# Kernel tuning notes

Hardware: AMD Instinct MI355X
Metric: run time of the kernel (lower is better)

## Reference

```python
import jax, jax.numpy as jnp
import numpy as np

INFTY_APPROX = 1e30
LAM = 10000.0


def sinusoid_embs(length, width):
    # Transformer-XL sinusoidal embeddings, flipped so row 0 encodes the
    # largest relative distance (length-1), matching the rel_shift convention.
    pos = jnp.arange(length, dtype=jnp.float32)
    inv_lams = 1.0 / (LAM ** (jnp.arange(0, width, 2, dtype=jnp.float32) / width))
    pre = pos[:, None] * inv_lams[None, :]                 # [T, width//2]
    cat = jnp.concatenate([jnp.sin(pre), jnp.cos(pre)], axis=-1)  # [T, width]
    return jnp.flip(cat, axis=0)


def rel_shift(x):
    # x: [B, T, T] -> out[b,i,j] = x[b, i, j - i + T - 1] (XL pad/reshape trick)
    b, t, _ = x.shape
    x = jnp.pad(x, ((0, 0), (0, 0), (1, 0)))               # [B, T, T+1]
    x = x.reshape(b, t + 1, t)[:, 1:, :]                   # [B, T, T]
    return x


def setup_inputs() -> dict:
    B, T, D, K, V = 2, 4096, 1024, 128, 2048
    key = jax.random.key(0)
    ks = jax.random.split(key, 10)
    s_d = 1.0 / np.sqrt(D)
    s_v = 1.0 / np.sqrt(V)
    return {
        'x':    jax.random.normal(ks[0], (B, T, D), dtype=jnp.float32),
        'g_ln': jnp.ones((D,), dtype=jnp.float32),
        'W_q':  s_d * jax.random.normal(ks[1], (D, K), dtype=jnp.float32),
        'W_k':  s_d * jax.random.normal(ks[2], (D, K), dtype=jnp.float32),
        'W_v':  s_d * jax.random.normal(ks[3], (D, V), dtype=jnp.float32),
        'W_g':  s_d * jax.random.normal(ks[4], (D, V), dtype=jnp.float32),
        'W_r':  s_d * jax.random.normal(ks[5], (D, K), dtype=jnp.float32),
        'xl_u': 0.02 * jax.random.normal(ks[6], (K,), dtype=jnp.float32),
        'xl_v': 0.02 * jax.random.normal(ks[7], (K,), dtype=jnp.float32),
        'W_o':  s_v * jax.random.normal(ks[8], (V, D), dtype=jnp.float32),
    }


def reference(x, g_ln, W_q, W_k, W_v, W_g, W_r, xl_u, xl_v, W_o):
    B, T, D = x.shape
    K = W_q.shape[-1]
    tau = jnp.asarray(K, x.dtype) ** 0.5

    # RMSNorm input layernorm
    x_tilde = x * jax.lax.rsqrt(jnp.mean(jnp.square(x), axis=-1, keepdims=True) + 1e-6)
    x_tilde = x_tilde * g_ln

    # QKVG projections; queries pre-scaled by 1/tau (producer-side scaling)
    q = (x_tilde @ W_q) / tau                              # [B, T, K]
    k = x_tilde @ W_k                                      # [B, T, K]
    v = x_tilde @ W_v                                      # [B, T, V]

    # XL relative-position bias inputs
    xl_r = sinusoid_embs(T, D) @ W_r                       # [T, K]

    # AC term (content) and BD term (position) with XL u/v biases
    scores_ac = jnp.einsum('bik,bjk->bij', q + xl_u, k)    # [B, T, T]
    scores_bd = jnp.einsum('bik,jk->bij', q + xl_v, xl_r)  # [B, T, T]
    scores_bd = rel_shift(scores_bd)

    scores = scores_ac + scores_bd
    keep = jnp.tril(jnp.ones((T, T), dtype=bool))          # causal keep mask
    scores = scores - jnp.asarray(INFTY_APPROX, x.dtype) * jnp.logical_not(keep)

    w = jax.nn.softmax(scores, axis=-1)                    # [B, T, T]
    wv = jnp.einsum('bij,bjv->biv', w, v)                  # [B, T, V]

    # SHGA gating (GAU-style silu gate)
    wv = wv * jax.nn.silu(x_tilde @ W_g)

    res = wv @ W_o                                         # [B, T, D]
    return res
```

## Files before the change

### kernel.cpp

```cpp
#include <hip/hip_runtime.h>
#include <hip/hip_bf16.h>
#include <stdint.h>

typedef __attribute__((ext_vector_type(4))) float f32x4;
typedef __attribute__((ext_vector_type(8))) short s16x8;
typedef __attribute__((ext_vector_type(8))) unsigned short u16x8;
typedef __attribute__((ext_vector_type(4))) unsigned short u16x4;

static __device__ __forceinline__ float b2f(unsigned short u) {
  union { unsigned int i; float f; } v; v.i = ((unsigned int)u) << 16; return v.f;
}
static __device__ __forceinline__ unsigned short f2b(float f) {
  unsigned int x = __float_as_uint(f);
  return (unsigned short)((x + 0x7fffu + ((x >> 16) & 1u)) >> 16);
}

typedef __attribute__((address_space(1))) const void gconst_t;
typedef __attribute__((address_space(3))) void lds_t;
static __device__ __forceinline__ void gload_lds16(const void* g, void* l) {
  __builtin_amdgcn_global_load_lds((gconst_t*)g, (lds_t*)l, 16, 0, 0);
}

template<int N>
static __device__ __forceinline__ void vmwait() {
  asm volatile("s_waitcnt vmcnt(%0)" :: "n"(N) : "memory");
}

struct GemmP {
  const unsigned short* A; const unsigned short* B; void* C;
  long sA, sB, sC;
  int M, N, K, lda, ldb, ldc;
  int causal, kend_mode;
  int gxs, gys, qchunk;
  const float* uvec; const float* vvec;
  unsigned short* qv_out; unsigned short* kk_out; float invtau;
  const float* rinv; const unsigned short* gate;
  const unsigned short* bds; float* stats;
};

template<int NREP, int EPI>
__launch_bounds__(512, 4)
__global__ void gemm2p_k(GemmP p) {
  constexpr int BN = NREP * 64;
  constexpr int CB = NREP / 2;
  constexpr int LPT = 1 + CB;
  const int lin = (int)blockIdx.x + (((int)blockIdx.y + (int)blockIdx.z * (int)gridDim.y) << p.gxs);
  const int wg = (lin & 7) * p.qchunk + (lin >> 3);
  int ii = wg & ((1 << p.gxs) - 1);
  const int jj = (wg >> p.gxs) & ((1 << p.gys) - 1);
  const int b  = wg >> (p.gxs + p.gys);
  if (p.kend_mode) ii = (1 << p.gxs) - 1 - ii;
  const int i0 = ii * 128, j0 = jj * BN;
  if (p.causal && j0 > i0 + 127) return;
  const unsigned short* Ag = p.A + (long)b * p.sA + (long)i0 * p.lda;
  const unsigned short* Bg = p.B + (long)b * p.sB + (long)j0 * p.ldb;
  const int kend = p.kend_mode ? min(p.K, i0 + 128) : p.K;
  const int NT = kend >> 5;

  __shared__ unsigned short As[3][128 * 32];
  __shared__ unsigned short Bs[3][BN * 32];

  const int tid = threadIdx.x;
  const int w = tid >> 6, l = tid & 63;
  const int wr = w >> 2, wc = w & 3;
  const int lrow = l >> 2;
  const int swz = ((l & 3) ^ ((l >> 3) & 3)) * 8;

  auto stage = [&](int t, int bi) {
    gload_lds16((const void*)(Ag + (long)(w * 16 + lrow) * p.lda + t * 32 + swz),
                (void*)(&As[bi][w * 512]));
#pragma unroll
    for (int i = 0; i < CB; ++i) {
      const int c = w * CB + i;
      gload_lds16((const void*)(Bg + (long)(c * 16 + lrow) * p.ldb + t * 32 + swz),
                  (void*)(&Bs[bi][c * 512]));
    }
  };

  f32x4 acc[4][NREP];
#pragma unroll
  for (int m = 0; m < 4; ++m)
#pragma unroll
    for (int n = 0; n < NREP; ++n) acc[m][n] = (f32x4){0.f, 0.f, 0.f, 0.f};

  const int fr = l & 15, fq = l >> 4;
  const int rg = (fq ^ ((fr >> 1) & 3)) * 8;
  const int aoff = (wr * 64 + fr) * 32 + rg;
  const int boff = (wc * (NREP * 16) + fr) * 32 + rg;

  stage(0, 0);
  if (NT > 1) stage(1, 1);

  int bi = 0;
  for (int t = 0; t < NT; ++t) {
    if (t == NT - 1) vmwait<0>(); else vmwait<LPT>();
    __builtin_amdgcn_s_barrier();
    __builtin_amdgcn_sched_barrier(0);
    const unsigned short* as = &As[bi][0];
    const unsigned short* bs = &Bs[bi][0];
    s16x8 af[4], bf[NREP];
#pragma unroll
    for (int m = 0; m < 4; ++m) af[m] = *(const s16x8*)(as + aoff + m * 512);
#pragma unroll
    for (int n = 0; n < NREP; ++n) bf[n] = *(const s16x8*)(bs + boff + n * 512);
    if (t + 2 < NT) {
      int bi2 = bi + 2; if (bi2 >= 3) bi2 -= 3;
      stage(t + 2, bi2);
    }
    __builtin_amdgcn_s_setprio(1);
#pragma unroll
    for (int m = 0; m < 4; ++m)
#pragma unroll
      for (int n = 0; n < NREP; ++n)
        acc[m][n] = __builtin_amdgcn_mfma_f32_16x16x32_bf16(af[m], bf[n], acc[m][n], 0, 0, 0);
    __builtin_amdgcn_s_setprio(0);
    bi = (bi + 1 == 3) ? 0 : bi + 1;
  }

  const int rbase = i0 + wr * 64 + fq * 4;
  const int cbase = j0 + wc * (NREP * 16) + fr;
  const long tb = (long)b * p.sC;

  if constexpr (EPI == 6) {
    float ps[16];
#pragma unroll
    for (int t = 0; t < 16; ++t) ps[t] = 0.f;
#pragma unroll
    for (int m = 0; m < 4; ++m) {
#pragma unroll
      for (int n = 0; n < NREP; ++n) {
        const int col = cbase + n * 16;
#pragma unroll
        for (int e = 0; e < 4; ++e) {
          const int row = rbase + m * 16 + e;
          const long o = tb + (long)row * p.ldc + col;
          float ev = 0.f;
          if (col <= row) {
            const float s = acc[m][n][e] + b2f(p.bds[o]);
            ev = __expf(fminf(s, 60.f));
          }
          ((unsigned short*)p.C)[o] = f2b(ev);
          ps[m * 4 + e] += ev;
        }
      }
    }
#pragma unroll
    for (int t = 0; t < 16; ++t) {
      float v = ps[t];
      v += __shfl_xor(v, 1); v += __shfl_xor(v, 2);
      v += __shfl_xor(v, 4); v += __shfl_xor(v, 8);
      ps[t] = v;
    }
    if (fr == 0) {
#pragma unroll
      for (int t = 0; t < 16; ++t) {
        const int row = rbase + (t >> 2) * 16 + (t & 3);
        p.stats[((long)(b * p.M + row) * 16 + jj) * 4 + wc] = ps[t];
      }
    }
    return;
  }

#pragma unroll
  for (int m = 0; m < 4; ++m) {
#pragma unroll
    for (int n = 0; n < NREP; ++n) {
      const int col = cbase + n * 16;
#pragma unroll
      for (int e = 0; e < 4; ++e) {
        const int row = rbase + m * 16 + e;
        const float val = acc[m][n][e];
        if constexpr (EPI == 0) {
          ((unsigned short*)p.C)[tb + (long)row * p.ldc + col] = f2b(val);
        } else if constexpr (EPI == 1) {
          ((float*)p.C)[tb + (long)row * p.ldc + col] = val;
        } else if constexpr (EPI == 2) {
          ((unsigned short*)p.C)[tb + (long)row * p.ldc + col] =
              f2b(val / (1.f + __expf(-val)));
        } else if constexpr (EPI == 4) {
          const long coff = tb + (long)row * p.ldc + col;
          const float g = b2f(p.gate[coff]);
          const float r = p.rinv[b * p.M + row];
          ((unsigned short*)p.C)[coff] = f2b(val * r * g);
        } else if constexpr (EPI == 5) {
          if (col <= row)
            ((unsigned short*)p.C)[tb + (long)row * p.ldc + (row - col)] = f2b(val);
        }
      }
    }
  }
}

template<int EPI>
__launch_bounds__(256)
__global__ void gemm_bt_k(GemmP p) {
  const int i0 = blockIdx.x * 128;
  const int j0 = blockIdx.y * 128;
  const int b  = blockIdx.z;
  const unsigned short* A = p.A + (long)b * p.sA + (long)i0 * p.lda;
  const unsigned short* B = p.B + (long)b * p.sB + (long)j0 * p.ldb;
  const int kend = p.K;

  __shared__ unsigned short As[128 * 32];
  __shared__ unsigned short Bs[128 * 32];

  const int tid = threadIdx.x;
  const int w = tid >> 6, l = tid & 63;
  const int wr = w >> 1, wc = w & 1;

  f32x4 acc[4][4];
#pragma unroll
  for (int m = 0; m < 4; ++m)
#pragma unroll
    for (int n = 0; n < 4; ++n) acc[m][n] = (f32x4){0.f, 0.f, 0.f, 0.f};

  const int srow = (l >> 2);
  const int scol = ((l & 3) ^ ((l >> 3) & 3)) * 8;
  const unsigned short* ga0 = A + (long)(w * 16 + srow) * p.lda + scol;
  const unsigned short* ga1 = A + (long)((w + 4) * 16 + srow) * p.lda + scol;
  const unsigned short* gb0 = B + (long)(w * 16 + srow) * p.ldb + scol;
  const unsigned short* gb1 = B + (long)((w + 4) * 16 + srow) * p.ldb + scol;
  unsigned short* la0 = As + w * 512;
  unsigned short* la1 = As + (w + 4) * 512;
  unsigned short* lb0 = Bs + w * 512;
  unsigned short* lb1 = Bs + (w + 4) * 512;

  const int rg = ((l >> 4) ^ (((l & 15) >> 1) & 3)) * 8;
  const unsigned short* ap = As + ((wr * 64) + (l & 15)) * 32 + rg;
  const unsigned short* bp = Bs + ((wc * 64) + (l & 15)) * 32 + rg;

  for (int k0 = 0; k0 < kend; k0 += 32) {
    gload_lds16(ga0 + k0, la0);
    gload_lds16(ga1 + k0, la1);
    gload_lds16(gb0 + k0, lb0);
    gload_lds16(gb1 + k0, lb1);
    __syncthreads();
    s16x8 af[4], bfr[4];
#pragma unroll
    for (int m = 0; m < 4; ++m) af[m] = *(const s16x8*)(ap + m * 16 * 32);
#pragma unroll
    for (int n = 0; n < 4; ++n) bfr[n] = *(const s16x8*)(bp + n * 16 * 32);
#pragma unroll
    for (int m = 0; m < 4; ++m)
#pragma unroll
      for (int n = 0; n < 4; ++n)
        acc[m][n] = __builtin_amdgcn_mfma_f32_16x16x32_bf16(af[m], bfr[n], acc[m][n], 0, 0, 0);
    __syncthreads();
  }

  const int rbase = i0 + wr * 64 + (l >> 4) * 4;
  const int cbase = j0 + wc * 64 + (l & 15);
#pragma unroll
  for (int m = 0; m < 4; ++m) {
#pragma unroll
    for (int n = 0; n < 4; ++n) {
      const int col = cbase + n * 16;
#pragma unroll
      for (int e = 0; e < 4; ++e) {
        const int row = rbase + m * 16 + e;
        const float val = acc[m][n][e];
        if constexpr (EPI == 0) {
          ((unsigned short*)p.C)[(long)b * p.sC + (long)row * p.ldc + col] = f2b(val);
        } else if constexpr (EPI == 3) {
          if (j0 == 0) {
            const float q = val * p.invtau;
            const long o = (long)row * 128 + col;
            ((unsigned short*)p.C)[o] = f2b(q + p.uvec[col]);
            p.qv_out[o] = f2b(q + p.vvec[col]);
          } else {
            p.kk_out[(long)row * 128 + (col - 128)] = f2b(val);
          }
        }
      }
    }
  }
}

__launch_bounds__(256)
__global__ void rmsnorm_k(const float* __restrict__ x, const float* __restrict__ g,
                          unsigned short* __restrict__ xt) {
  const long row = blockIdx.x;
  const float* xr = x + row * 1024;
  const int t = threadIdx.x;
  const float4 v = ((const float4*)xr)[t];
  float ss = v.x * v.x + v.y * v.y + v.z * v.z + v.w * v.w;
#pragma unroll
  for (int o = 1; o < 64; o <<= 1) ss += __shfl_xor(ss, o);
  __shared__ float wsum[4];
  if ((t & 63) == 0) wsum[t >> 6] = ss;
  __syncthreads();
  const float tot = wsum[0] + wsum[1] + wsum[2] + wsum[3];
  const float r = 1.0f / sqrtf(tot * (1.0f / 1024.0f) + 1e-6f);
  const float4 gv = ((const float4*)g)[t];
  u16x4 o;
  o.x = f2b(v.x * r * gv.x); o.y = f2b(v.y * r * gv.y);
  o.z = f2b(v.z * r * gv.z); o.w = f2b(v.w * r * gv.w);
  ((u16x4*)(xt + row * 1024))[t] = o;
}

__launch_bounds__(256)
__global__ void sinemb_k(unsigned short* __restrict__ emb) {
  const int idx = blockIdx.x * 256 + threadIdx.x;
  const int t = idx >> 10, w = idx & 1023;
  const int h = w & 511;
  const float inv = __expf(-(float)h * (9.2103403719761836f / 512.0f));
  const float pre = (float)t * inv;
  const float val = (w < 512) ? sinf(pre) : cosf(pre);
  emb[idx] = f2b(val);
}

__launch_bounds__(256)
__global__ void transcast_k(const float* __restrict__ in, unsigned short* __restrict__ out,
                            int R, int C) {
  __shared__ float tile[32][33];
  const int c0 = blockIdx.x * 32, r0 = blockIdx.y * 32;
  const int tx = threadIdx.x & 31, ty = threadIdx.x >> 5;
#pragma unroll
  for (int k = 0; k < 4; ++k)
    tile[ty + k * 8][tx] = in[(long)(r0 + ty + k * 8) * C + c0 + tx];
  __syncthreads();
#pragma unroll
  for (int k = 0; k < 4; ++k)
    out[(long)(c0 + ty + k * 8) * R + r0 + tx] = f2b(tile[tx][ty + k * 8]);
}

__global__ void rowinv_k(const float* __restrict__ stats, float* __restrict__ rinv,
                         int T, int BT) {
  const int idx = blockIdx.x * 256 + threadIdx.x;
  if (idx >= BT) return;
  const int i = idx & (T - 1);
  const int nt = (i >> 8) + 1;
  const float* st = stats + (long)idx * 64;
  float s = 0.f;
  for (int jt = 0; jt < nt; ++jt)
    s += st[jt * 4] + st[jt * 4 + 1] + st[jt * 4 + 2] + st[jt * 4 + 3];
  rinv[idx] = 1.0f / s;
}

extern "C" void kernel_launch(void* const* d_in, const int* in_sizes, int n_in,
                              void* d_out, int out_size, void* d_ws, size_t ws_size,
                              hipStream_t stream) {
  const float* x    = (const float*)d_in[0];
  const float* g_ln = (const float*)d_in[1];
  const float* W_q  = (const float*)d_in[2];
  const float* W_k  = (const float*)d_in[3];
  const float* W_v  = (const float*)d_in[4];
  const float* W_g  = (const float*)d_in[5];
  const float* W_r  = (const float*)d_in[6];
  const float* xl_u = (const float*)d_in[7];
  const float* xl_v = (const float*)d_in[8];
  const float* W_o  = (const float*)d_in[9];
  float* out = (float*)d_out;

  const int B = 2, T = 4096, D = 1024, K = 128, V = 2048;
  const int BT = B * T;

  char* ws = (char*)d_ws;
  size_t off = 0;
  auto alloc = [&](size_t bytes) -> void* {
    void* p = ws + off; off += (bytes + 255) & ~(size_t)255; return p;
  };
  unsigned short* XT   = (unsigned short*)alloc((size_t)BT * D * 2);
  unsigned short* WQKT = (unsigned short*)alloc((size_t)256 * D * 2);
  unsigned short* WVT  = (unsigned short*)alloc((size_t)V * D * 2);
  unsigned short* WGT  = (unsigned short*)alloc((size_t)V * D * 2);
  unsigned short* WRT  = (unsigned short*)alloc((size_t)K * D * 2);
  unsigned short* WOT  = (unsigned short*)alloc((size_t)D * V * 2);
  unsigned short* QU   = (unsigned short*)alloc((size_t)BT * K * 2);
  unsigned short* QV   = (unsigned short*)alloc((size_t)BT * K * 2);
  unsigned short* KKb  = (unsigned short*)alloc((size_t)BT * K * 2);
  unsigned short* RR   = (unsigned short*)alloc((size_t)T * K * 2);
  unsigned short* VVT  = (unsigned short*)alloc((size_t)V * BT * 2);
  unsigned short* GATE = (unsigned short*)alloc((size_t)BT * V * 2);
  float* STATS         = (float*)alloc((size_t)BT * 64 * 4);
  float* RINV          = (float*)alloc((size_t)BT * 4);
  unsigned short* EBUF = (unsigned short*)alloc((size_t)B * T * T * 2);
  unsigned short* BD2  = (unsigned short*)alloc((size_t)B * T * T * 2);
  unsigned short* EMB  = BD2;
  unsigned short* WVG  = BD2;
  if (off > ws_size) return;
  (void)in_sizes; (void)n_in; (void)out_size;

  const float invtau = 0.08838834764831845f;

  transcast_k<<<dim3(K / 32, D / 32), 256, 0, stream>>>(W_q, WQKT, D, K);
  transcast_k<<<dim3(K / 32, D / 32), 256, 0, stream>>>(W_k, WQKT + (size_t)K * D, D, K);
  transcast_k<<<dim3(V / 32, D / 32), 256, 0, stream>>>(W_v, WVT, D, V);
  transcast_k<<<dim3(V / 32, D / 32), 256, 0, stream>>>(W_g, WGT, D, V);
  transcast_k<<<dim3(K / 32, D / 32), 256, 0, stream>>>(W_r, WRT, D, K);
  transcast_k<<<dim3(D / 32, V / 32), 256, 0, stream>>>(W_o, WOT, V, D);
  rmsnorm_k<<<BT, 256, 0, stream>>>(x, g_ln, XT);
  sinemb_k<<<(T * D) / 256, 256, 0, stream>>>(EMB);

  {
    GemmP p{}; p.A = XT; p.B = WQKT; p.C = QU;
    p.M = BT; p.N = 256; p.K = D; p.lda = D; p.ldb = D; p.ldc = K;
    p.uvec = xl_u; p.vvec = xl_v; p.qv_out = QV; p.kk_out = KKb; p.invtau = invtau;
    gemm_bt_k<3><<<dim3(BT / 128, 2, 1), 256, 0, stream>>>(p);
  }
  {
    GemmP p{}; p.A = EMB; p.B = WRT; p.C = RR;
    p.M = T; p.N = K; p.K = D; p.lda = D; p.ldb = D; p.ldc = K;
    gemm_bt_k<0><<<dim3(T / 128, 1, 1), 256, 0, stream>>>(p);
  }
  {
    GemmP p{}; p.A = WVT; p.B = XT; p.C = VVT;
    p.M = V; p.N = BT; p.K = D; p.lda = D; p.ldb = D; p.ldc = BT;
    p.gxs = 4; p.gys = 5; p.qchunk = 64;
    gemm2p_k<4, 0><<<dim3(16, 32, 1), 512, 0, stream>>>(p);
  }
  {
    GemmP p{}; p.A = XT; p.B = WGT; p.C = GATE;
    p.M = BT; p.N = V; p.K = D; p.lda = D; p.ldb = D; p.ldc = V;
    p.gxs = 6; p.gys = 3; p.qchunk = 64;
    gemm2p_k<4, 2><<<dim3(64, 8, 1), 512, 0, stream>>>(p);
  }
  {
    GemmP p{}; p.A = QV; p.B = RR; p.C = BD2;
    p.sA = (long)T * K; p.sB = 0; p.sC = (long)T * T;
    p.M = T; p.N = T; p.K = K; p.lda = K; p.ldb = K; p.ldc = T; p.causal = 1;
    p.gxs = 5; p.gys = 4; p.qchunk = 128;
    gemm2p_k<4, 5><<<dim3(32, 16, B), 512, 0, stream>>>(p);
  }
  {
    GemmP p{}; p.A = QU; p.B = KKb; p.C = EBUF;
    p.sA = (long)T * K; p.sB = (long)T * K; p.sC = (long)T * T;
    p.M = T; p.N = T; p.K = K; p.lda = K; p.ldb = K; p.ldc = T; p.causal = 1;
    p.bds = BD2; p.stats = STATS;
    p.gxs = 5; p.gys = 4; p.qchunk = 128;
    gemm2p_k<4, 6><<<dim3(32, 16, B), 512, 0, stream>>>(p);
  }
  rowinv_k<<<BT / 256, 256, 0, stream>>>(STATS, RINV, T, BT);
  {
    GemmP p{}; p.A = EBUF; p.B = VVT; p.C = WVG;
    p.sA = (long)T * T; p.sB = T; p.sC = (long)T * V;
    p.M = T; p.N = V; p.K = T; p.lda = T; p.ldb = BT; p.ldc = V;
    p.kend_mode = 1; p.rinv = RINV; p.gate = GATE;
    p.gxs = 5; p.gys = 3; p.qchunk = 64;
    gemm2p_k<4, 4><<<dim3(32, 8, B), 512, 0, stream>>>(p);
  }
  {
    GemmP p{}; p.A = WVG; p.B = WOT; p.C = out;
    p.M = BT; p.N = D; p.K = V; p.lda = V; p.ldb = V; p.ldc = D;
    p.gxs = 6; p.gys = 3; p.qchunk = 64;
    gemm2p_k<2, 1><<<dim3(64, 8, 1), 512, 0, stream>>>(p);
  }
}
```

Measured before the change: 408.8 us.

## Add larger-tile 4-stage pipelined GEMM kernel for V, gate, PV and output projections

```diff
diff --git a/kernel.cpp b/kernel.cpp
--- a/kernel.cpp
+++ b/kernel.cpp
@@ -24,6 +24,10 @@
 template<int N>
 static __device__ __forceinline__ void vmwait() {
   asm volatile("s_waitcnt vmcnt(%0)" :: "n"(N) : "memory");
+}
+static __device__ __forceinline__ void lgkm0() {
+  asm volatile("s_waitcnt lgkmcnt(0)" ::: "memory");
+  __builtin_amdgcn_sched_barrier(0);
 }
 
 struct GemmP {
@@ -37,6 +41,145 @@
   const float* rinv; const unsigned short* gate;
   const unsigned short* bds; float* stats;
 };
+
+template<int WM, int WN, int MFR, int NFR, int EPI>
+__launch_bounds__(512, 2)
+__global__ void gemm3_k(GemmP p) {
+  constexpr int BM = WM * MFR * 16;
+  constexpr int BN = WN * NFR * 16;
+  constexpr int LA = BM / 128;
+  constexpr int LB = BN / 128;
+  constexpr int LPT = LA + LB;
+  const int lin = (int)blockIdx.x + (((int)blockIdx.y + (int)blockIdx.z * (int)gridDim.y) << p.gxs);
+  const int wg = (lin & 7) * p.qchunk + (lin >> 3);
+  int ii = wg & ((1 << p.gxs) - 1);
+  const int jj = (wg >> p.gxs) & ((1 << p.gys) - 1);
+  const int b  = wg >> (p.gxs + p.gys);
+  if (p.kend_mode) ii = (1 << p.gxs) - 1 - ii;
+  const int i0 = ii * BM, j0 = jj * BN;
+  const unsigned short* Ag = p.A + (long)b * p.sA + (long)i0 * p.lda;
+  const unsigned short* Bg = p.B + (long)b * p.sB + (long)j0 * p.ldb;
+  const int kend = p.kend_mode ? min(p.K, i0 + BM) : p.K;
+  const int NT = kend >> 5;
+
+  __shared__ unsigned short As[4][BM * 32];
+  __shared__ unsigned short Bs[4][BN * 32];
+
+  const int tid = threadIdx.x;
+  const int w = tid >> 6, l = tid & 63;
+  const int wr = w / WN, wc = w % WN;
+
+  auto stageA = [&](int t, int s) {
+#pragma unroll
+    for (int j = 0; j < LA; ++j) {
+      const int sl = j * 512 + tid;
+      const int r = sl >> 2, g = sl & 3;
+      gload_lds16((const void*)(Ag + (long)r * p.lda + t * 32 + ((g ^ ((r >> 1) & 3)) << 3)),
+                  (void*)(&As[s][sl << 3]));
+    }
+  };
+  auto stageB = [&](int t, int s) {
+#pragma unroll
+    for (int j = 0; j < LB; ++j) {
+      const int sl = j * 512 + tid;
+      const int r = sl >> 2, g = sl & 3;
+      gload_lds16((const void*)(Bg + (long)r * p.ldb + t * 32 + ((g ^ ((r >> 1) & 3)) << 3)),
+                  (void*)(&Bs[s][sl << 3]));
+    }
+  };
+
+  f32x4 acc[MFR][NFR];
+#pragma unroll
+  for (int m = 0; m < MFR; ++m)
+#pragma unroll
+    for (int n = 0; n < NFR; ++n) acc[m][n] = (f32x4){0.f, 0.f, 0.f, 0.f};
+
+  const int fr = l & 15, fq = l >> 4;
+  const int rg = (fq ^ ((fr >> 1) & 3)) << 3;
+  const int aoff = (wr * (MFR * 16) + fr) * 32 + rg;
+  const int boff = (wc * (NFR * 16) + fr) * 32 + rg;
+
+  if (NT > 0) { stageA(0, 0); stageB(0, 0); }
+  if (NT > 1) { stageA(1, 1); stageB(1, 1); }
+  if (NT > 2) { stageA(2, 2); stageB(2, 2); }
+
+  constexpr int H = (MFR == 8) ? 4 : MFR;
+
+  for (int t = 0; t < NT; ++t) {
+    const int s = t & 3;
+    const int rem = NT - 1 - t;
+    if (rem >= 2)      vmwait<2 * LPT>();
+    else if (rem == 1) vmwait<LPT>();
+    else               vmwait<0>();
+    __builtin_amdgcn_s_barrier();
+    __builtin_amdgcn_sched_barrier(0);
+    const unsigned short* as = &As[s][0];
+    const unsigned short* bs = &Bs[s][0];
+    const int s3 = (t + 3) & 3;
+    const bool pf = (t + 3 < NT);
+
+    s16x8 bf[NFR];
+#pragma unroll
+    for (int n = 0; n < NFR; ++n) bf[n] = *(const s16x8*)(bs + boff + n * 512);
+    s16x8 af0[H];
+#pragma unroll
+    for (int m = 0; m < H; ++m) af0[m] = *(const s16x8*)(as + aoff + m * 512);
+    if (pf) stageA(t + 3, s3);
+    if constexpr (MFR != 8) { if (pf) stageB(t + 3, s3); }
+    lgkm0();
+    __builtin_amdgcn_s_setprio(1);
+#pragma unroll
+    for (int m = 0; m < H; ++m)
+#pragma unroll
+      for (int n = 0; n < NFR; ++n)
+        acc[m][n] = __builtin_amdgcn_mfma_f32_16x16x32_bf16(af0[m], bf[n], acc[m][n], 0, 0, 0);
+    __builtin_amdgcn_s_setprio(0);
+
+    if constexpr (MFR == 8) {
+      s16x8 af1[4];
+#pragma unroll
+      for (int m = 0; m < 4; ++m) af1[m] = *(const s16x8*)(as + aoff + (m + 4) * 512);
+      if (pf) stageB(t + 3, s3);
+      lgkm0();
+      __builtin_amdgcn_s_setprio(1);
+#pragma unroll
+      for (int m = 0; m < 4; ++m)
+#pragma unroll
+        for (int n = 0; n < NFR; ++n)
+          acc[m + 4][n] = __builtin_amdgcn_mfma_f32_16x16x32_bf16(af1[m], bf[n], acc[m + 4][n], 0, 0, 0);
+      __builtin_amdgcn_s_setprio(0);
+    }
+  }
+
+  const int rbase = i0 + wr * (MFR * 16) + fq * 4;
+  const int cbase = j0 + wc * (NFR * 16) + fr;
+  const long tb = (long)b * p.sC;
+#pragma unroll
+  for (int m = 0; m < MFR; ++m) {
+#pragma unroll
+    for (int n = 0; n < NFR; ++n) {
+      const int col = cbase + n * 16;
+#pragma unroll
+      for (int e = 0; e < 4; ++e) {
+        const int row = rbase + m * 16 + e;
+        const float val = acc[m][n][e];
+        if constexpr (EPI == 0) {
+          ((unsigned short*)p.C)[tb + (long)row * p.ldc + col] = f2b(val);
+        } else if constexpr (EPI == 1) {
+          ((float*)p.C)[tb + (long)row * p.ldc + col] = val;
+        } else if constexpr (EPI == 2) {
+          ((unsigned short*)p.C)[tb + (long)row * p.ldc + col] =
+              f2b(val / (1.f + __expf(-val)));
+        } else if constexpr (EPI == 4) {
+          const long coff = tb + (long)row * p.ldc + col;
+          const float g = b2f(p.gate[coff]);
+          const float r = p.rinv[b * p.M + row];
+          ((unsigned short*)p.C)[coff] = f2b(val * r * g);
+        }
+      }
+    }
+  }
+}
 
 template<int NREP, int EPI>
 __launch_bounds__(512, 4)
@@ -170,19 +313,7 @@
       for (int e = 0; e < 4; ++e) {
         const int row = rbase + m * 16 + e;
         const float val = acc[m][n][e];
-        if constexpr (EPI == 0) {
-          ((unsigned short*)p.C)[tb + (long)row * p.ldc + col] = f2b(val);
-        } else if constexpr (EPI == 1) {
-          ((float*)p.C)[tb + (long)row * p.ldc + col] = val;
-        } else if constexpr (EPI == 2) {
-          ((unsigned short*)p.C)[tb + (long)row * p.ldc + col] =
-              f2b(val / (1.f + __expf(-val)));
-        } else if constexpr (EPI == 4) {
-          const long coff = tb + (long)row * p.ldc + col;
-          const float g = b2f(p.gate[coff]);
-          const float r = p.rinv[b * p.M + row];
-          ((unsigned short*)p.C)[coff] = f2b(val * r * g);
-        } else if constexpr (EPI == 5) {
+        if constexpr (EPI == 5) {
           if (col <= row)
             ((unsigned short*)p.C)[tb + (long)row * p.ldc + (row - col)] = f2b(val);
         }
@@ -406,14 +537,14 @@
   {
     GemmP p{}; p.A = WVT; p.B = XT; p.C = VVT;
     p.M = V; p.N = BT; p.K = D; p.lda = D; p.ldb = D; p.ldc = BT;
-    p.gxs = 4; p.gys = 5; p.qchunk = 64;
-    gemm2p_k<4, 0><<<dim3(16, 32, 1), 512, 0, stream>>>(p);
+    p.gxs = 3; p.gys = 5; p.qchunk = 32;
+    gemm3_k<2, 4, 8, 4, 0><<<dim3(8, 32, 1), 512, 0, stream>>>(p);
   }
   {
     GemmP p{}; p.A = XT; p.B = WGT; p.C = GATE;
     p.M = BT; p.N = V; p.K = D; p.lda = D; p.ldb = D; p.ldc = V;
-    p.gxs = 6; p.gys = 3; p.qchunk = 64;
-    gemm2p_k<4, 2><<<dim3(64, 8, 1), 512, 0, stream>>>(p);
+    p.gxs = 5; p.gys = 3; p.qchunk = 32;
+    gemm3_k<2, 4, 8, 4, 2><<<dim3(32, 8, 1), 512, 0, stream>>>(p);
   }
   {
     GemmP p{}; p.A = QV; p.B = RR; p.C = BD2;
@@ -436,13 +567,13 @@
     p.sA = (long)T * T; p.sB = T; p.sC = (long)T * V;
     p.M = T; p.N = V; p.K = T; p.lda = T; p.ldb = BT; p.ldc = V;
     p.kend_mode = 1; p.rinv = RINV; p.gate = GATE;
-    p.gxs = 5; p.gys = 3; p.qchunk = 64;
-    gemm2p_k<4, 4><<<dim3(32, 8, B), 512, 0, stream>>>(p);
+    p.gxs = 4; p.gys = 4; p.qchunk = 64;
+    gemm3_k<4, 2, 4, 4, 4><<<dim3(16, 16, B), 512, 0, stream>>>(p);
   }
   {
     GemmP p{}; p.A = WVG; p.B = WOT; p.C = out;
     p.M = BT; p.N = D; p.K = V; p.lda = V; p.ldb = V; p.ldc = D;
-    p.gxs = 6; p.gys = 3; p.qchunk = 64;
-    gemm2p_k<2, 1><<<dim3(64, 8, 1), 512, 0, stream>>>(p);
-  }
-}
+    p.gxs = 5; p.gys = 3; p.qchunk = 32;
+    gemm3_k<4, 2, 4, 4, 1><<<dim3(32, 8, 1), 512, 0, stream>>>(p);
+  }
+}
```

After: 461.6 us. 12.9% more time.

## Add 8-wave 256-tile GEMM kernels with paired causal row blocks for projections and PV

Applied to the files above, without the earlier changes.

```diff
diff --git a/kernel.cpp b/kernel.cpp
--- a/kernel.cpp
+++ b/kernel.cpp
@@ -25,18 +25,288 @@
 static __device__ __forceinline__ void vmwait() {
   asm volatile("s_waitcnt vmcnt(%0)" :: "n"(N) : "memory");
 }
+static __device__ __forceinline__ void barmid() {
+  __builtin_amdgcn_sched_barrier(0);
+  __builtin_amdgcn_s_barrier();
+  asm volatile("s_waitcnt lgkmcnt(0)" ::: "memory");
+  __builtin_amdgcn_sched_barrier(0);
+}
+static __device__ __forceinline__ void barend() {
+  __builtin_amdgcn_sched_barrier(0);
+  __builtin_amdgcn_s_barrier();
+}
 
 struct GemmP {
   const unsigned short* A; const unsigned short* B; void* C;
   long sA, sB, sC;
   int M, N, K, lda, ldb, ldc;
-  int causal, kend_mode;
+  int causal, kend_mode, swapxy;
   int gxs, gys, qchunk;
   const float* uvec; const float* vvec;
   unsigned short* qv_out; unsigned short* kk_out; float invtau;
   const float* rinv; const unsigned short* gate;
   const unsigned short* bds; float* stats;
 };
+
+template<int EPI>
+__launch_bounds__(512, 2)
+__global__ void gemm8p256_k(GemmP p) {
+  __shared__ unsigned short L[2][4][8192];
+  const int lin = (int)blockIdx.x + (int)gridDim.x * ((int)blockIdx.y + (int)gridDim.y * (int)blockIdx.z);
+  const int wg = (lin & 7) * p.qchunk + (lin >> 3);
+  const int xx = wg & ((1 << p.gxs) - 1);
+  const int yy = (wg >> p.gxs) & ((1 << p.gys) - 1);
+  const int ii = p.swapxy ? yy : xx;
+  const int jj = p.swapxy ? xx : yy;
+  const int i0 = ii * 256, j0 = jj * 256;
+  const unsigned short* Ag = p.A + (long)i0 * p.lda;
+  const unsigned short* Bg = p.B + (long)j0 * p.ldb;
+  const int lda = p.lda, ldb = p.ldb;
+  const int NI = p.K >> 7;
+
+  const int tid = threadIdx.x;
+  const int w = tid >> 6, l = tid & 63;
+  const int wr = w >> 2, wc = w & 3;
+  const int fr = l & 15, fq = l >> 4;
+
+  auto stA = [&](int slot, int h, int t) {
+#pragma unroll
+    for (int u = 0; u < 2; ++u) {
+      const int sl = u * 512 + tid, r = sl >> 3, g = sl & 7;
+      const int gs = g ^ (((r >> 2) & 1) << 1);
+      gload_lds16(Ag + (long)(h * 128 + r) * lda + t * 64 + gs * 8, &L[slot][h][sl * 8]);
+    }
+  };
+  auto stB = [&](int slot, int h, int t) {
+#pragma unroll
+    for (int u = 0; u < 2; ++u) {
+      const int sl = u * 512 + tid, r = sl >> 3, g = sl & 7;
+      const int gs = g ^ (((r >> 2) & 1) << 1);
+      gload_lds16(Bg + (long)(h * 128 + r) * ldb + t * 64 + gs * 8, &L[slot][2 + h][sl * 8]);
+    }
+  };
+
+  f32x4 acc[8][4];
+#pragma unroll
+  for (int m = 0; m < 8; ++m)
+#pragma unroll
+    for (int n = 0; n < 4; ++n) acc[m][n] = (f32x4){0.f, 0.f, 0.f, 0.f};
+
+  const int abase = (((fr << 7) + (fq << 4)) ^ ((fr & 4) << 3));
+  const int bbase = ((((wc & 1) << 13) + (fr << 7) + (fq << 4)) ^ ((fr & 4) << 3));
+  s16x8 a[4][2], bA[2][2], bB[2][2];
+
+  auto rdA = [&](int slot, int mq) {
+#pragma unroll
+    for (int m = 0; m < 4; ++m)
+#pragma unroll
+      for (int ks = 0; ks < 2; ++ks)
+        a[m][ks] = *(const s16x8*)((const char*)&L[slot][wr][0] +
+                                   (abase | ((mq * 4 + m) << 11) | (ks << 6)));
+  };
+  auto rdB = [&](int slot, int nq, s16x8 (&bb)[2][2]) {
+    const int reg = 2 + (wc >> 1);
+#pragma unroll
+    for (int n = 0; n < 2; ++n)
+#pragma unroll
+      for (int ks = 0; ks < 2; ++ks)
+        bb[n][ks] = *(const s16x8*)((const char*)&L[slot][reg][0] +
+                                    (bbase | ((nq * 2 + n) << 11) | (ks << 6)));
+  };
+  auto mm = [&](int mq, int nq, s16x8 (&bb)[2][2]) {
+    __builtin_amdgcn_s_setprio(1);
+#pragma unroll
+    for (int m = 0; m < 4; ++m)
+#pragma unroll
+      for (int n = 0; n < 2; ++n)
+#pragma unroll
+        for (int ks = 0; ks < 2; ++ks)
+          acc[mq * 4 + m][nq * 2 + n] =
+              __builtin_amdgcn_mfma_f32_16x16x32_bf16(a[m][ks], bb[n][ks],
+                                                      acc[mq * 4 + m][nq * 2 + n], 0, 0, 0);
+    __builtin_amdgcn_s_setprio(0);
+  };
+
+  stB(0, 0, 0); stB(0, 1, 0); stA(0, 0, 0); stA(0, 1, 0);
+  stB(1, 0, 1); stB(1, 1, 1);
+  vmwait<4>();
+  barend();
+
+  for (int it = 0; it < NI; ++it) {
+    const int t0 = 2 * it, t1 = t0 + 1;
+    const bool lastI = (it == NI - 1);
+    rdA(0, 0); rdB(0, 0, bA); stA(1, 0, t1);
+    barmid(); mm(0, 0, bA); barend();
+    rdB(0, 1, bB); stA(1, 1, t1);
+    barmid(); mm(0, 1, bB); barend();
+    rdA(0, 1);
+    if (!lastI) stB(0, 0, t0 + 2);
+    barmid(); mm(1, 1, bB); barend();
+    if (!lastI) stB(0, 1, t0 + 2);
+    barmid(); mm(1, 0, bA);
+    if (lastI) vmwait<0>(); else vmwait<4>();
+    barend();
+    rdA(1, 0); rdB(1, 0, bA);
+    if (!lastI) stA(0, 0, t0 + 2);
+    barmid(); mm(0, 0, bA); barend();
+    rdB(1, 1, bB);
+    if (!lastI) stA(0, 1, t0 + 2);
+    barmid(); mm(0, 1, bB); barend();
+    rdA(1, 1);
+    if (!lastI) stB(1, 0, t1 + 2);
+    barmid(); mm(1, 1, bB); barend();
+    if (!lastI) stB(1, 1, t1 + 2);
+    barmid(); mm(1, 0, bA);
+    if (!lastI) vmwait<4>();
+    barend();
+  }
+
+  const int rb = i0 + wr * 128 + fq * 4;
+  const int cb = j0 + wc * 64 + fr;
+#pragma unroll
+  for (int m = 0; m < 8; ++m)
+#pragma unroll
+    for (int n = 0; n < 4; ++n) {
+      const int col = cb + n * 16;
+#pragma unroll
+      for (int e = 0; e < 4; ++e) {
+        const int row = rb + m * 16 + e;
+        const float val = acc[m][n][e];
+        if constexpr (EPI == 0)
+          ((unsigned short*)p.C)[(long)row * p.ldc + col] = f2b(val);
+        else
+          ((unsigned short*)p.C)[(long)row * p.ldc + col] = f2b(val / (1.f + __expf(-val)));
+      }
+    }
+}
+
+template<int PAIR, int EPI>
+__launch_bounds__(512, 2)
+__global__ void gemm8p128_k(GemmP p) {
+  __shared__ unsigned short L[3][3][8192];
+  const int lin = (int)blockIdx.x + (int)gridDim.x * ((int)blockIdx.y + (int)gridDim.y * (int)blockIdx.z);
+  const int wg = (lin & 7) * p.qchunk + (lin >> 3);
+  const int xx = wg & ((1 << p.gxs) - 1);
+  const int yy = (wg >> p.gxs) & ((1 << p.gys) - 1);
+  const int b  = wg >> (p.gxs + p.gys);
+  const int jj = PAIR ? yy : (p.swapxy ? xx : yy);
+  const int j0 = jj * 128;
+  const unsigned short* Bg0 = p.B + (long)b * p.sB + (long)j0 * p.ldb;
+  const int lda = p.lda, ldb = p.ldb;
+
+  const int tid = threadIdx.x;
+  const int w = tid >> 6, l = tid & 63;
+  const int wr = w >> 1, wc = w & 1;
+  const int fr = l & 15, fq = l >> 4;
+
+  const int abase = ((((wr & 1) << 13) + (fr << 7) + (fq << 4)) ^ ((fr & 4) << 3));
+  const int bbase = (((wc << 13) + (fr << 7) + (fq << 4)) ^ ((fr & 4) << 3));
+
+  const int passes = PAIR ? 2 : 1;
+  for (int ps = 0; ps < passes; ++ps) {
+    const int ii = PAIR ? (ps ? xx : (15 - xx)) : (p.swapxy ? yy : xx);
+    const int i0 = ii * 256;
+    const unsigned short* Ag = p.A + (long)b * p.sA + (long)i0 * lda;
+    const int kend = p.kend_mode ? min(p.K, i0 + 256) : p.K;
+    const int NT = kend >> 6;
+
+    auto stA = [&](int slot, int h, int t) {
+#pragma unroll
+      for (int u = 0; u < 2; ++u) {
+        const int sl = u * 512 + tid, r = sl >> 3, g = sl & 7;
+        const int gs = g ^ (((r >> 2) & 1) << 1);
+        gload_lds16(Ag + (long)(h * 128 + r) * lda + t * 64 + gs * 8, &L[slot][h][sl * 8]);
+      }
+    };
+    auto stB = [&](int slot, int bh, int t) {
+      const int r = tid >> 3, g = tid & 7;
+      const int rloc = bh * 64 + r;
+      const int gs = g ^ (((rloc >> 2) & 1) << 1);
+      gload_lds16(Bg0 + (long)rloc * ldb + t * 64 + gs * 8, &L[slot][2][bh * 4096 + tid * 8]);
+    };
+
+    f32x4 acc[4][4];
+#pragma unroll
+    for (int m = 0; m < 4; ++m)
+#pragma unroll
+      for (int n = 0; n < 4; ++n) acc[m][n] = (f32x4){0.f, 0.f, 0.f, 0.f};
+    s16x8 a[4][2], bA[2][2], bB[2][2];
+
+    auto rdA = [&](int slot) {
+      const int reg = wr >> 1;
+#pragma unroll
+      for (int m = 0; m < 4; ++m)
+#pragma unroll
+        for (int ks = 0; ks < 2; ++ks)
+          a[m][ks] = *(const s16x8*)((const char*)&L[slot][reg][0] +
+                                     (abase | (m << 11) | (ks << 6)));
+    };
+    auto rdB = [&](int slot, int nq, s16x8 (&bb)[2][2]) {
+#pragma unroll
+      for (int n = 0; n < 2; ++n)
+#pragma unroll
+        for (int ks = 0; ks < 2; ++ks)
+          bb[n][ks] = *(const s16x8*)((const char*)&L[slot][2][0] +
+                                      (bbase | ((nq * 2 + n) << 11) | (ks << 6)));
+    };
+    auto mm = [&](int nq, s16x8 (&bb)[2][2]) {
+      __builtin_amdgcn_s_setprio(1);
+#pragma unroll
+      for (int m = 0; m < 4; ++m)
+#pragma unroll
+        for (int n = 0; n < 2; ++n)
+#pragma unroll
+          for (int ks = 0; ks < 2; ++ks)
+            acc[m][nq * 2 + n] =
+                __builtin_amdgcn_mfma_f32_16x16x32_bf16(a[m][ks], bb[n][ks],
+                                                        acc[m][nq * 2 + n], 0, 0, 0);
+      __builtin_amdgcn_s_setprio(0);
+    };
+
+    stA(0, 0, 0); stB(0, 0, 0); stA(0, 1, 0); stB(0, 1, 0);
+    stA(1, 0, 1); stB(1, 0, 1); stA(1, 1, 1); stB(1, 1, 1);
+    vmwait<6>();
+    barend();
+
+    int s = 0;
+    for (int t = 0; t < NT; ++t) {
+      int s2 = s + 2; if (s2 >= 3) s2 -= 3;
+      const bool pf = (t + 2 < NT);
+      rdA(s); rdB(s, 0, bA);
+      if (pf) { stA(s2, 0, t + 2); stB(s2, 0, t + 2); }
+      barmid(); mm(0, bA); barend();
+      rdB(s, 1, bB);
+      if (pf) { stA(s2, 1, t + 2); stB(s2, 1, t + 2); }
+      barmid(); mm(1, bB);
+      if (t == NT - 2) vmwait<0>(); else if (t < NT - 2) vmwait<6>();
+      barend();
+      s = (s + 1 == 3) ? 0 : s + 1;
+    }
+
+    const int rb = i0 + wr * 64 + fq * 4;
+    const int cb = j0 + wc * 64 + fr;
+    const long tb = (long)b * p.sC;
+#pragma unroll
+    for (int m = 0; m < 4; ++m)
+#pragma unroll
+      for (int n = 0; n < 4; ++n) {
+        const int col = cb + n * 16;
+#pragma unroll
+        for (int e = 0; e < 4; ++e) {
+          const int row = rb + m * 16 + e;
+          const float val = acc[m][n][e];
+          if constexpr (EPI == 1) {
+            ((float*)p.C)[tb + (long)row * p.ldc + col] = val;
+          } else {
+            const long coff = tb + (long)row * p.ldc + col;
+            const float g = b2f(p.gate[coff]);
+            const float r = p.rinv[b * p.M + row];
+            ((unsigned short*)p.C)[coff] = f2b(val * r * g);
+          }
+        }
+      }
+  }
+}
 
 template<int NREP, int EPI>
 __launch_bounds__(512, 4)
@@ -46,16 +316,14 @@
   constexpr int LPT = 1 + CB;
   const int lin = (int)blockIdx.x + (((int)blockIdx.y + (int)blockIdx.z * (int)gridDim.y) << p.gxs);
   const int wg = (lin & 7) * p.qchunk + (lin >> 3);
-  int ii = wg & ((1 << p.gxs) - 1);
+  const int ii = wg & ((1 << p.gxs) - 1);
   const int jj = (wg >> p.gxs) & ((1 << p.gys) - 1);
   const int b  = wg >> (p.gxs + p.gys);
-  if (p.kend_mode) ii = (1 << p.gxs) - 1 - ii;
   const int i0 = ii * 128, j0 = jj * BN;
   if (p.causal && j0 > i0 + 127) return;
   const unsigned short* Ag = p.A + (long)b * p.sA + (long)i0 * p.lda;
   const unsigned short* Bg = p.B + (long)b * p.sB + (long)j0 * p.ldb;
-  const int kend = p.kend_mode ? min(p.K, i0 + 128) : p.K;
-  const int NT = kend >> 5;
+  const int NT = p.K >> 5;
 
   __shared__ unsigned short As[3][128 * 32];
   __shared__ unsigned short Bs[3][BN * 32];
@@ -67,13 +335,11 @@
   const int swz = ((l & 3) ^ ((l >> 3) & 3)) * 8;
 
   auto stage = [&](int t, int bi) {
-    gload_lds16((const void*)(Ag + (long)(w * 16 + lrow) * p.lda + t * 32 + swz),
-                (void*)(&As[bi][w * 512]));
+    gload_lds16(Ag + (long)(w * 16 + lrow) * p.lda + t * 32 + swz, &As[bi][w * 512]);
 #pragma unroll
     for (int i = 0; i < CB; ++i) {
       const int c = w * CB + i;
-      gload_lds16((const void*)(Bg + (long)(c * 16 + lrow) * p.ldb + t * 32 + swz),
-                  (void*)(&Bs[bi][c * 512]));
+      gload_lds16(Bg + (long)(c * 16 + lrow) * p.ldb + t * 32 + swz, &Bs[bi][c * 512]);
     }
   };
 
@@ -122,11 +388,11 @@
   const long tb = (long)b * p.sC;
 
   if constexpr (EPI == 6) {
-    float ps[16];
-#pragma unroll
-    for (int t = 0; t < 16; ++t) ps[t] = 0.f;
-#pragma unroll
-    for (int m = 0; m < 4; ++m) {
+    float psum[16];
+#pragma unroll
+    for (int t = 0; t < 16; ++t) psum[t] = 0.f;
+#pragma unroll
+    for (int m = 0; m < 4; ++m)
 #pragma unroll
       for (int n = 0; n < NREP; ++n) {
         const int col = cbase + n * 16;
@@ -140,55 +406,40 @@
             ev = __expf(fminf(s, 60.f));
           }
           ((unsigned short*)p.C)[o] = f2b(ev);
-          ps[m * 4 + e] += ev;
+          psum[m * 4 + e] += ev;
         }
       }
-    }
 #pragma unroll
     for (int t = 0; t < 16; ++t) {
-      float v = ps[t];
+      float v = psum[t];
       v += __shfl_xor(v, 1); v += __shfl_xor(v, 2);
       v += __shfl_xor(v, 4); v += __shfl_xor(v, 8);
-      ps[t] = v;
+      psum[t] = v;
     }
     if (fr == 0) {
 #pragma unroll
       for (int t = 0; t < 16; ++t) {
         const int row = rbase + (t >> 2) * 16 + (t & 3);
-        p.stats[((long)(b * p.M + row) * 16 + jj) * 4 + wc] = ps[t];
+        p.stats[((long)(b * p.M + row) * 16 + jj) * 4 + wc] = psum[t];
       }
     }
     return;
   }
 
 #pragma unroll
-  for (int m = 0; m < 4; ++m) {
+  for (int m = 0; m < 4; ++m)
 #pragma unroll
     for (int n = 0; n < NREP; ++n) {
       const int col = cbase + n * 16;
 #pragma unroll
       for (int e = 0; e < 4; ++e) {
         const int row = rbase + m * 16 + e;
-        const float val = acc[m][n][e];
-        if constexpr (EPI == 0) {
-          ((unsigned short*)p.C)[tb + (long)row * p.ldc + col] = f2b(val);
-        } else if constexpr (EPI == 1) {
-          ((float*)p.C)[tb + (long)row * p.ldc + col] = val;
-        } else if constexpr (EPI == 2) {
-          ((unsigned short*)p.C)[tb + (long)row * p.ldc + col] =
-              f2b(val / (1.f + __expf(-val)));
-        } else if constexpr (EPI == 4) {
-          const long coff = tb + (long)row * p.ldc + col;
-          const float g = b2f(p.gate[coff]);
-          const float r = p.rinv[b * p.M + row];
-          ((unsigned short*)p.C)[coff] = f2b(val * r * g);
-        } else if constexpr (EPI == 5) {
+        if constexpr (EPI == 5) {
           if (col <= row)
-            ((unsigned short*)p.C)[tb + (long)row * p.ldc + (row - col)] = f2b(val);
+            ((unsigned short*)p.C)[tb + (long)row * p.ldc + (row - col)] = f2b(acc[m][n][e]);
         }
       }
     }
-  }
 }
 
 template<int EPI>
@@ -196,10 +447,8 @@
 __global__ void gemm_bt_k(GemmP p) {
   const int i0 = blockIdx.x * 128;
   const int j0 = blockIdx.y * 128;
-  const int b  = blockIdx.z;
-  const unsigned short* A = p.A + (long)b * p.sA + (long)i0 * p.lda;
-  const unsigned short* B = p.B + (long)b * p.sB + (long)j0 * p.ldb;
-  const int kend = p.K;
+  const unsigned short* A = p.A + (long)i0 * p.lda;
+  const unsigned short* B = p.B + (long)j0 * p.ldb;
 
   __shared__ unsigned short As[128 * 32];
   __shared__ unsigned short Bs[128 * 32];
@@ -229,7 +478,7 @@
   const unsigned short* ap = As + ((wr * 64) + (l & 15)) * 32 + rg;
   const unsigned short* bp = Bs + ((wc * 64) + (l & 15)) * 32 + rg;
 
-  for (int k0 = 0; k0 < kend; k0 += 32) {
+  for (int k0 = 0; k0 < p.K; k0 += 32) {
     gload_lds16(ga0 + k0, la0);
     gload_lds16(ga1 + k0, la1);
     gload_lds16(gb0 + k0, lb0);
@@ -251,7 +500,7 @@
   const int rbase = i0 + wr * 64 + (l >> 4) * 4;
   const int cbase = j0 + wc * 64 + (l & 15);
 #pragma unroll
-  for (int m = 0; m < 4; ++m) {
+  for (int m = 0; m < 4; ++m)
 #pragma unroll
     for (int n = 0; n < 4; ++n) {
       const int col = cbase + n * 16;
@@ -260,7 +509,7 @@
         const int row = rbase + m * 16 + e;
         const float val = acc[m][n][e];
         if constexpr (EPI == 0) {
-          ((unsigned short*)p.C)[(long)b * p.sC + (long)row * p.ldc + col] = f2b(val);
+          ((unsigned short*)p.C)[(long)row * p.ldc + col] = f2b(val);
         } else if constexpr (EPI == 3) {
           if (j0 == 0) {
             const float q = val * p.invtau;
@@ -273,7 +522,6 @@
         }
       }
     }
-  }
 }
 
 __launch_bounds__(256)
@@ -406,14 +654,14 @@
   {
     GemmP p{}; p.A = WVT; p.B = XT; p.C = VVT;
     p.M = V; p.N = BT; p.K = D; p.lda = D; p.ldb = D; p.ldc = BT;
-    p.gxs = 4; p.gys = 5; p.qchunk = 64;
-    gemm2p_k<4, 0><<<dim3(16, 32, 1), 512, 0, stream>>>(p);
+    p.gxs = 3; p.gys = 5; p.qchunk = 32; p.swapxy = 0;
+    gemm8p256_k<0><<<dim3(8, 32, 1), 512, 0, stream>>>(p);
   }
   {
     GemmP p{}; p.A = XT; p.B = WGT; p.C = GATE;
     p.M = BT; p.N = V; p.K = D; p.lda = D; p.ldb = D; p.ldc = V;
-    p.gxs = 6; p.gys = 3; p.qchunk = 64;
-    gemm2p_k<4, 2><<<dim3(64, 8, 1), 512, 0, stream>>>(p);
+    p.gxs = 3; p.gys = 5; p.qchunk = 32; p.swapxy = 1;
+    gemm8p256_k<2><<<dim3(8, 32, 1), 512, 0, stream>>>(p);
   }
   {
     GemmP p{}; p.A = QV; p.B = RR; p.C = BD2;
@@ -436,13 +684,13 @@
     p.sA = (long)T * T; p.sB = T; p.sC = (long)T * V;
     p.M = T; p.N = V; p.K = T; p.lda = T; p.ldb = BT; p.ldc = V;
     p.kend_mode = 1; p.rinv = RINV; p.gate = GATE;
-    p.gxs = 5; p.gys = 3; p.qchunk = 64;
-    gemm2p_k<4, 4><<<dim3(32, 8, B), 512, 0, stream>>>(p);
+    p.gxs = 3; p.gys = 4; p.qchunk = 32;
+    gemm8p128_k<1, 4><<<dim3(8, 16, 2), 512, 0, stream>>>(p);
   }
   {
     GemmP p{}; p.A = WVG; p.B = WOT; p.C = out;
     p.M = BT; p.N = D; p.K = V; p.lda = V; p.ldb = V; p.ldc = D;
-    p.gxs = 6; p.gys = 3; p.qchunk = 64;
-    gemm2p_k<2, 1><<<dim3(64, 8, 1), 512, 0, stream>>>(p);
-  }
-}
+    p.gxs = 3; p.gys = 5; p.qchunk = 32; p.swapxy = 1;
+    gemm8p128_k<0, 1><<<dim3(8, 32, 1), 512, 0, stream>>>(p);
+  }
+}
```

Result: slower. 433.0 us (+5.9%).
